# Optimization experiments

Measured on AMD Instinct MI355X. Metric: run time of the kernel, lower is better.

## Reference

```python
import jax, jax.numpy as jnp
import numpy as np

EXTENTS = (1, 1, 1)
DIM = 256
HEADS = 8
DH = 32
INNER = HEADS * DH
SCALE = DH ** -0.5
NEG = -1e9


def _windows(t):
    """t: (B, S, H, W, C) -> (B, S, H, W, K, C) local 3D windows, K = prod(2e+1).
    Pads with zeros, window dims flattened in (s, h, w) order (matches unfold i j k)."""
    e = EXTENTS
    B, S, H, W, C = t.shape
    tp = jnp.pad(t, [(0, 0), (e[0], e[0]), (e[1], e[1]), (e[2], e[2]), (0, 0)])
    slabs = []
    for dz in range(2 * e[0] + 1):
        for dy in range(2 * e[1] + 1):
            for dx in range(2 * e[2] + 1):
                slabs.append(tp[:, dz:dz + S, dy:dy + H, dx:dx + W, :])
    return jnp.stack(slabs, axis=4)


def setup_inputs() -> dict:
    key = jax.random.key(0)
    ks = jax.random.split(key, 8)
    B, S, H, W = 2, 8, 32, 32
    scale_w = DIM ** -0.5
    return {
        "x": jax.random.normal(ks[0], (B, S, H, W, DIM), jnp.float32),
        "q": jax.random.normal(ks[1], (B, S, H, W, DIM), jnp.float32),
        "Wq": jax.random.normal(ks[2], (DIM, INNER), jnp.float32) * scale_w,
        "Wk": jax.random.normal(ks[3], (DIM, INNER), jnp.float32) * scale_w,
        "Wv": jax.random.normal(ks[4], (DIM, INNER), jnp.float32) * scale_w,
        "bv": jax.random.normal(ks[5], (INNER,), jnp.float32) * 0.02,
        "Wo": jax.random.normal(ks[6], (INNER, DIM), jnp.float32) * (INNER ** -0.5),
        "bo": jax.random.normal(ks[7], (DIM,), jnp.float32) * 0.02,
    }


def reference(x, q, Wq, Wk, Wv, bv, Wo, bo):
    B, S, H, W, _ = x.shape
    k = x @ Wk                      # (B,S,H,W,INNER)
    v = x @ Wv + bv
    qp = q @ Wq

    kw = _windows(k)                # (B,S,H,W,K,INNER)
    vw = _windows(v)
    K = kw.shape[4]

    # mask: True where window element falls on padding (out of bounds)
    valid = _windows(jnp.ones((1, S, H, W, 1), jnp.float32))[..., 0] > 0  # (1,S,H,W,K)
    mask = ~valid

    qh = qp.reshape(B, S, H, W, HEADS, DH)
    kh = kw.reshape(B, S, H, W, K, HEADS, DH)
    vh = vw.reshape(B, S, H, W, K, HEADS, DH)

    dots = jnp.einsum('bshwnd,bshwknd->bshwnk', qh, kh) * SCALE  # (B,S,H,W,HEADS,K)
    dots = jnp.where(mask[:, :, :, :, None, :], NEG, dots)
    attn = jax.nn.softmax(dots, axis=-1)
    out = jnp.einsum('bshwnk,bshwknd->bshwnd', attn, vh)
    out = out.reshape(B, S, H, W, INNER)
    return out @ Wo + bo            # (B,S,H,W,DIM)
```

## Files before the change

kernel.cpp:

```cpp
#include <hip/hip_runtime.h>
#include <hip/hip_bf16.h>
#include <math.h>

#define B_N 2
#define S_N 8
#define H_N 32
#define W_N 32
#define DIM_N 256
#define NPOS (B_N * S_N * H_N * W_N)
#define NP (NPOS * DIM_N)
#define SCALE_F 0.1767766952966369f

typedef __attribute__((ext_vector_type(8))) short bf16x8;
typedef __attribute__((ext_vector_type(4))) float f32x4;

__device__ __forceinline__ unsigned short f2b(float f) {
    __hip_bfloat16 h = __float2bfloat16(f);
    return __builtin_bit_cast(unsigned short, h);
}
__device__ __forceinline__ unsigned pk2(float a, float b) {
    return (unsigned)f2b(a) | ((unsigned)f2b(b) << 16);
}
__device__ __forceinline__ float bl(unsigned u) { return __uint_as_float(u << 16); }
__device__ __forceinline__ float bh(unsigned u) { return __uint_as_float(u & 0xffff0000u); }

__global__ __launch_bounds__(256)
void wtrans_kernel(const float* __restrict__ Wq, const float* __restrict__ Wk,
                   const float* __restrict__ Wv, const float* __restrict__ Wo,
                   unsigned short* __restrict__ wt)
{
    int mat = blockIdx.y;
    const float* W = (mat == 0) ? Wq : (mat == 1) ? Wk : (mat == 2) ? Wv : Wo;
    unsigned short* Wt = wt + (size_t)mat * 65536;
    int tile = blockIdx.x;
    int tk = tile >> 3, tn = tile & 7;
    __shared__ float t[32][33];
    int c = threadIdx.x & 31;
    int r0 = (threadIdx.x >> 5) * 4;
#pragma unroll
    for (int i = 0; i < 4; ++i)
        t[r0 + i][c] = W[(size_t)(tk * 32 + r0 + i) * 256 + tn * 32 + c];
    __syncthreads();
#pragma unroll
    for (int i = 0; i < 4; ++i)
        Wt[(size_t)(tn * 32 + r0 + i) * 256 + tk * 32 + c] = f2b(t[c][r0 + i]);
}

template<bool A_F32, bool OUT_HM>
__device__ __forceinline__ void gemm_body(
    const void* __restrict__ Aptr, const unsigned short* __restrict__ Wt,
    const float* __restrict__ bias, unsigned short* __restrict__ out_hm,
    float* __restrict__ out_f, int row0, int col0)
{
    __shared__ unsigned short Al[128][72];
    __shared__ unsigned short Bl[128][72];

    const int tid = threadIdx.x;
    const int lane = tid & 63;
    const int wid = tid >> 6;
    const int wr = wid >> 1, wc = wid & 1;
    const int l15 = lane & 15, l4 = lane >> 4;

    f32x4 acc[4][4];
#pragma unroll
    for (int m = 0; m < 4; ++m)
#pragma unroll
        for (int n = 0; n < 4; ++n) acc[m][n] = (f32x4){0.f, 0.f, 0.f, 0.f};

    const int r = tid >> 3, s = tid & 7;

    for (int kt = 0; kt < DIM_N; kt += 64) {
#pragma unroll
        for (int j = 0; j < 4; ++j) {
            int rr = r + j * 32;
            if (A_F32) {
                const float* Af = (const float*)Aptr;
                const float* p = &Af[(size_t)(row0 + rr) * DIM_N + kt + s * 8];
                float4 f0 = *(const float4*)p;
                float4 f1 = *(const float4*)(p + 4);
                uint4 va;
                va.x = pk2(f0.x, f0.y); va.y = pk2(f0.z, f0.w);
                va.z = pk2(f1.x, f1.y); va.w = pk2(f1.z, f1.w);
                *(uint4*)&Al[rr][s * 8] = va;
            } else {
                const unsigned short* Ab = (const unsigned short*)Aptr;
                *(uint4*)&Al[rr][s * 8] =
                    *(const uint4*)&Ab[(size_t)(row0 + rr) * DIM_N + kt + s * 8];
            }
            *(uint4*)&Bl[rr][s * 8] =
                *(const uint4*)&Wt[(size_t)(col0 + rr) * DIM_N + kt + s * 8];
        }
        __syncthreads();
#pragma unroll
        for (int ks = 0; ks < 2; ++ks) {
            bf16x8 af[4], bfr[4];
#pragma unroll
            for (int m = 0; m < 4; ++m)
                af[m] = *(const bf16x8*)&Al[wr * 64 + m * 16 + l15][ks * 32 + l4 * 8];
#pragma unroll
            for (int n = 0; n < 4; ++n)
                bfr[n] = *(const bf16x8*)&Bl[wc * 64 + n * 16 + l15][ks * 32 + l4 * 8];
#pragma unroll
            for (int m = 0; m < 4; ++m)
#pragma unroll
                for (int n = 0; n < 4; ++n)
                    acc[m][n] = __builtin_amdgcn_mfma_f32_16x16x32_bf16(
                        af[m], bfr[n], acc[m][n], 0, 0, 0);
        }
        __syncthreads();
    }

    const int rowb = row0 + wr * 64 + l4 * 4;
    const int colb = col0 + wc * 64 + l15;
#pragma unroll
    for (int n = 0; n < 4; ++n) {
        int col = colb + n * 16;
        float bb = bias ? bias[col] : 0.f;
        int head = col >> 5, dh = col & 31;
#pragma unroll
        for (int m = 0; m < 4; ++m) {
#pragma unroll
            for (int rg = 0; rg < 4; ++rg) {
                int row = rowb + m * 16 + rg;
                float v = acc[m][n][rg] + bb;
                if (OUT_HM)
                    out_hm[((size_t)head * NPOS + row) * 32 + dh] = f2b(v);
                else
                    out_f[(size_t)row * DIM_N + col] = v;
            }
        }
    }
}

__global__ __launch_bounds__(256, 2)
void proj_mfma(const float* __restrict__ x, const float* __restrict__ q,
               const unsigned short* __restrict__ wt, const float* __restrict__ bv,
               unsigned short* __restrict__ qhb, unsigned short* __restrict__ khb,
               unsigned short* __restrict__ vhb)
{
    int z = blockIdx.z;
    const float* A = (z == 0) ? q : x;
    const unsigned short* W = wt + (size_t)z * 65536;
    unsigned short* out = (z == 0) ? qhb : (z == 1) ? khb : vhb;
    const float* bias = (z == 2) ? bv : nullptr;
    gemm_body<true, true>(A, W, bias, out, nullptr, blockIdx.x * 128, blockIdx.y * 128);
}

__global__ __launch_bounds__(256, 2)
void outp_mfma(const unsigned short* __restrict__ ao, const unsigned short* __restrict__ wt,
               const float* __restrict__ bo, float* __restrict__ out)
{
    gemm_body<false, false>(ao, wt + 3 * 65536, bo, nullptr, out,
                            blockIdx.x * 128, blockIdx.y * 128);
}

__global__ __launch_bounds__(256, 2)
void attn_kernel(const unsigned short* __restrict__ qh, const unsigned short* __restrict__ kh,
                 const unsigned short* __restrict__ vh, unsigned short* __restrict__ aop)
{
    __shared__ unsigned short aol[32 * 256];

    int bix = blockIdx.x;
    int h = bix & 31, s = (bix >> 5) & 7, b = bix >> 8;
    int n = threadIdx.x >> 5;
    int w = threadIdx.x & 31;

    size_t rowbase = (((size_t)b * S_N + s) * H_N + h) * W_N;
    size_t pos = rowbase + w;
    const unsigned short* qrow = qh + ((size_t)n * NPOS + pos) * 32;
    float qv[32];
#pragma unroll
    for (int j = 0; j < 4; ++j) {
        uint4 u = ((const uint4*)qrow)[j];
        qv[j * 8 + 0] = bl(u.x); qv[j * 8 + 1] = bh(u.x);
        qv[j * 8 + 2] = bl(u.y); qv[j * 8 + 3] = bh(u.y);
        qv[j * 8 + 4] = bl(u.z); qv[j * 8 + 5] = bh(u.z);
        qv[j * 8 + 6] = bl(u.w); qv[j * 8 + 7] = bh(u.w);
    }

    float dots[27];
#pragma unroll
    for (int dz = 0; dz < 3; ++dz)
#pragma unroll
        for (int dy = 0; dy < 3; ++dy)
#pragma unroll
            for (int dx = 0; dx < 3; ++dx) {
                int idx = (dz * 3 + dy) * 3 + dx;
                int ns = s + dz - 1, nh = h + dy - 1, nw = w + dx - 1;
                bool ok = (unsigned)ns < S_N && (unsigned)nh < H_N &&
                          (unsigned)nw < W_N;
                float d = -1e30f;
                if (ok) {
                    size_t np = (((size_t)b * S_N + ns) * H_N + nh) * W_N + nw;
                    const unsigned short* krow = kh + ((size_t)n * NPOS + np) * 32;
                    float acc = 0.f;
#pragma unroll
                    for (int j = 0; j < 4; ++j) {
                        uint4 u = ((const uint4*)krow)[j];
                        acc = fmaf(qv[j * 8 + 0], bl(u.x), acc);
                        acc = fmaf(qv[j * 8 + 1], bh(u.x), acc);
                        acc = fmaf(qv[j * 8 + 2], bl(u.y), acc);
                        acc = fmaf(qv[j * 8 + 3], bh(u.y), acc);
                        acc = fmaf(qv[j * 8 + 4], bl(u.z), acc);
                        acc = fmaf(qv[j * 8 + 5], bh(u.z), acc);
                        acc = fmaf(qv[j * 8 + 6], bl(u.w), acc);
                        acc = fmaf(qv[j * 8 + 7], bh(u.w), acc);
                    }
                    d = acc * SCALE_F;
                }
                dots[idx] = d;
            }

    float m = dots[0];
#pragma unroll
    for (int i = 1; i < 27; ++i) m = fmaxf(m, dots[i]);
    float den = 0.f;
#pragma unroll
    for (int i = 0; i < 27; ++i) {
        float p = __expf(dots[i] - m);
        dots[i] = p;
        den += p;
    }
    float inv = 1.f / den;

    float ov[32];
#pragma unroll
    for (int i = 0; i < 32; ++i) ov[i] = 0.f;
#pragma unroll
    for (int dz = 0; dz < 3; ++dz)
#pragma unroll
        for (int dy = 0; dy < 3; ++dy)
#pragma unroll
            for (int dx = 0; dx < 3; ++dx) {
                int idx = (dz * 3 + dy) * 3 + dx;
                int ns = s + dz - 1, nh = h + dy - 1, nw = w + dx - 1;
                bool ok = (unsigned)ns < S_N && (unsigned)nh < H_N &&
                          (unsigned)nw < W_N;
                if (ok) {
                    size_t np = (((size_t)b * S_N + ns) * H_N + nh) * W_N + nw;
                    const unsigned short* vrow = vh + ((size_t)n * NPOS + np) * 32;
                    float p = dots[idx];
#pragma unroll
                    for (int j = 0; j < 4; ++j) {
                        uint4 u = ((const uint4*)vrow)[j];
                        ov[j * 8 + 0] = fmaf(p, bl(u.x), ov[j * 8 + 0]);
                        ov[j * 8 + 1] = fmaf(p, bh(u.x), ov[j * 8 + 1]);
                        ov[j * 8 + 2] = fmaf(p, bl(u.y), ov[j * 8 + 2]);
                        ov[j * 8 + 3] = fmaf(p, bh(u.y), ov[j * 8 + 3]);
                        ov[j * 8 + 4] = fmaf(p, bl(u.z), ov[j * 8 + 4]);
                        ov[j * 8 + 5] = fmaf(p, bh(u.z), ov[j * 8 + 5]);
                        ov[j * 8 + 6] = fmaf(p, bl(u.w), ov[j * 8 + 6]);
                        ov[j * 8 + 7] = fmaf(p, bh(u.w), ov[j * 8 + 7]);
                    }
                }
            }

#pragma unroll
    for (int j = 0; j < 4; ++j) {
        uint4 o;
        o.x = pk2(ov[j * 8 + 0] * inv, ov[j * 8 + 1] * inv);
        o.y = pk2(ov[j * 8 + 2] * inv, ov[j * 8 + 3] * inv);
        o.z = pk2(ov[j * 8 + 4] * inv, ov[j * 8 + 5] * inv);
        o.w = pk2(ov[j * 8 + 6] * inv, ov[j * 8 + 7] * inv);
        int unit = n * 4 + j;
        int su = unit ^ (w & 7);
        *(uint4*)&aol[w * 256 + su * 8] = o;
    }
    __syncthreads();
    int wrr = threadIdx.x >> 3, c = threadIdx.x & 7;
    size_t orow = rowbase + wrr;
#pragma unroll
    for (int u = 0; u < 4; ++u) {
        int unit = c * 4 + u;
        int su = unit ^ (wrr & 7);
        uint4 v = *(const uint4*)&aol[wrr * 256 + su * 8];
        ((uint4*)(aop + orow * 256))[unit] = v;
    }
}

extern "C" void kernel_launch(void* const* d_in, const int* in_sizes, int n_in,
                              void* d_out, int out_size, void* d_ws, size_t ws_size,
                              hipStream_t stream)
{
    const float* xin = (const float*)d_in[0];
    const float* qin = (const float*)d_in[1];
    const float* Wq  = (const float*)d_in[2];
    const float* Wk  = (const float*)d_in[3];
    const float* Wv  = (const float*)d_in[4];
    const float* bv  = (const float*)d_in[5];
    const float* Wo  = (const float*)d_in[6];
    const float* bo  = (const float*)d_in[7];
    float* out = (float*)d_out;

    unsigned short* ws = (unsigned short*)d_ws;
    unsigned short* wt = ws;
    unsigned short* qh = wt + (size_t)4 * 65536;
    unsigned short* kh = qh + (size_t)NP;
    unsigned short* vh = kh + (size_t)NP;
    unsigned short* ao = vh + (size_t)NP;

    dim3 gw(64, 4);
    wtrans_kernel<<<gw, 256, 0, stream>>>(Wq, Wk, Wv, Wo, wt);

    dim3 gp(NPOS / 128, DIM_N / 128, 3);
    proj_mfma<<<gp, 256, 0, stream>>>(xin, qin, wt, bv, qh, kh, vh);

    attn_kernel<<<B_N * S_N * H_N, 256, 0, stream>>>(qh, kh, vh, ao);

    dim3 go(NPOS / 128, DIM_N / 128, 1);
    outp_mfma<<<go, 256, 0, stream>>>(ao, wt, bo, out);
}
```

Before: 73.66 us.

## Fuse output projection into attention kernel and retile QKV projection GEMM

The output projection GEMM now runs inside the attention kernel. Each block multiplies its 32x256 bf16 attention tile, already held in shared memory, by Wo, staged tile by tile into LDS, and writes the fp32 result directly. This removes the intermediate attention-output buffer round trip through global memory and one kernel launch. The QKV projection is retiled to 64-row by full-256-column blocks with 512 threads, so each A row is converted once per block. The cost is that every attention block reloads all of Wo and now needs more LDS.

```diff
diff --git a/kernel.cpp b/kernel.cpp
--- a/kernel.cpp
+++ b/kernel.cpp
@@ -46,62 +46,66 @@
         Wt[(size_t)(tn * 32 + r0 + i) * 256 + tk * 32 + c] = f2b(t[c][r0 + i]);
 }
 
-template<bool A_F32, bool OUT_HM>
-__device__ __forceinline__ void gemm_body(
-    const void* __restrict__ Aptr, const unsigned short* __restrict__ Wt,
-    const float* __restrict__ bias, unsigned short* __restrict__ out_hm,
-    float* __restrict__ out_f, int row0, int col0)
+__global__ __launch_bounds__(512, 4)
+void proj_mfma(const float* __restrict__ x, const float* __restrict__ q,
+               const unsigned short* __restrict__ wt, const float* __restrict__ bv,
+               unsigned short* __restrict__ qh, unsigned short* __restrict__ kh,
+               unsigned short* __restrict__ vh)
 {
-    __shared__ unsigned short Al[128][72];
-    __shared__ unsigned short Bl[128][72];
+    __shared__ unsigned short Al[64][72];
+    __shared__ unsigned short Bl[256][72];
+
+    const int bx = blockIdx.x;
+    const int z = bx >> 8;
+    const int row0 = (bx & 255) * 64;
+    const float* A = (z == 0) ? q : x;
+    const unsigned short* Wtm = wt + (size_t)z * 65536;
+    unsigned short* outp = (z == 0) ? qh : (z == 1) ? kh : vh;
+    const float* bias = (z == 2) ? bv : nullptr;
 
     const int tid = threadIdx.x;
     const int lane = tid & 63;
     const int wid = tid >> 6;
-    const int wr = wid >> 1, wc = wid & 1;
+    const int wm = wid >> 2, wn = wid & 3;
     const int l15 = lane & 15, l4 = lane >> 4;
 
-    f32x4 acc[4][4];
-#pragma unroll
-    for (int m = 0; m < 4; ++m)
+    f32x4 acc[2][4];
+#pragma unroll
+    for (int m = 0; m < 2; ++m)
 #pragma unroll
         for (int n = 0; n < 4; ++n) acc[m][n] = (f32x4){0.f, 0.f, 0.f, 0.f};
 
-    const int r = tid >> 3, s = tid & 7;
+    const int ar = tid >> 3, as = tid & 7;
 
     for (int kt = 0; kt < DIM_N; kt += 64) {
-#pragma unroll
-        for (int j = 0; j < 4; ++j) {
-            int rr = r + j * 32;
-            if (A_F32) {
-                const float* Af = (const float*)Aptr;
-                const float* p = &Af[(size_t)(row0 + rr) * DIM_N + kt + s * 8];
-                float4 f0 = *(const float4*)p;
-                float4 f1 = *(const float4*)(p + 4);
-                uint4 va;
-                va.x = pk2(f0.x, f0.y); va.y = pk2(f0.z, f0.w);
-                va.z = pk2(f1.x, f1.y); va.w = pk2(f1.z, f1.w);
-                *(uint4*)&Al[rr][s * 8] = va;
-            } else {
-                const unsigned short* Ab = (const unsigned short*)Aptr;
-                *(uint4*)&Al[rr][s * 8] =
-                    *(const uint4*)&Ab[(size_t)(row0 + rr) * DIM_N + kt + s * 8];
-            }
-            *(uint4*)&Bl[rr][s * 8] =
-                *(const uint4*)&Wt[(size_t)(col0 + rr) * DIM_N + kt + s * 8];
+        {
+            const float* p = &A[(size_t)(row0 + ar) * DIM_N + kt + as * 8];
+            float4 f0 = *(const float4*)p;
+            float4 f1 = *(const float4*)(p + 4);
+            uint4 va;
+            va.x = pk2(f0.x, f0.y); va.y = pk2(f0.z, f0.w);
+            va.z = pk2(f1.x, f1.y); va.w = pk2(f1.z, f1.w);
+            *(uint4*)&Al[ar][as * 8] = va;
+        }
+#pragma unroll
+        for (int i = 0; i < 4; ++i) {
+            int u = tid + i * 512;
+            int rowb = u >> 3, su = u & 7;
+            *(uint4*)&Bl[rowb][su * 8] =
+                *(const uint4*)&Wtm[(size_t)rowb * DIM_N + kt + su * 8];
         }
         __syncthreads();
 #pragma unroll
         for (int ks = 0; ks < 2; ++ks) {
-            bf16x8 af[4], bfr[4];
-#pragma unroll
-            for (int m = 0; m < 4; ++m)
-                af[m] = *(const bf16x8*)&Al[wr * 64 + m * 16 + l15][ks * 32 + l4 * 8];
+            bf16x8 af[2], bfr[4];
+#pragma unroll
+            for (int m = 0; m < 2; ++m)
+                af[m] = *(const bf16x8*)&Al[wm * 32 + m * 16 + l15][ks * 32 + l4 * 8];
 #pragma unroll
             for (int n = 0; n < 4; ++n)
-                bfr[n] = *(const bf16x8*)&Bl[wc * 64 + n * 16 + l15][ks * 32 + l4 * 8];
-#pragma unroll
-            for (int m = 0; m < 4; ++m)
+                bfr[n] = *(const bf16x8*)&Bl[wn * 64 + n * 16 + l15][ks * 32 + l4 * 8];
+#pragma unroll
+            for (int m = 0; m < 2; ++m)
 #pragma unroll
                 for (int n = 0; n < 4; ++n)
                     acc[m][n] = __builtin_amdgcn_mfma_f32_16x16x32_bf16(
@@ -110,55 +114,30 @@
         __syncthreads();
     }
 
-    const int rowb = row0 + wr * 64 + l4 * 4;
-    const int colb = col0 + wc * 64 + l15;
 #pragma unroll
     for (int n = 0; n < 4; ++n) {
-        int col = colb + n * 16;
+        int col = wn * 64 + n * 16 + l15;
         float bb = bias ? bias[col] : 0.f;
         int head = col >> 5, dh = col & 31;
 #pragma unroll
-        for (int m = 0; m < 4; ++m) {
+        for (int m = 0; m < 2; ++m) {
 #pragma unroll
             for (int rg = 0; rg < 4; ++rg) {
-                int row = rowb + m * 16 + rg;
-                float v = acc[m][n][rg] + bb;
-                if (OUT_HM)
-                    out_hm[((size_t)head * NPOS + row) * 32 + dh] = f2b(v);
-                else
-                    out_f[(size_t)row * DIM_N + col] = v;
-            }
-        }
-    }
-}
-
-__global__ __launch_bounds__(256, 2)
-void proj_mfma(const float* __restrict__ x, const float* __restrict__ q,
-               const unsigned short* __restrict__ wt, const float* __restrict__ bv,
-               unsigned short* __restrict__ qhb, unsigned short* __restrict__ khb,
-               unsigned short* __restrict__ vhb)
-{
-    int z = blockIdx.z;
-    const float* A = (z == 0) ? q : x;
-    const unsigned short* W = wt + (size_t)z * 65536;
-    unsigned short* out = (z == 0) ? qhb : (z == 1) ? khb : vhb;
-    const float* bias = (z == 2) ? bv : nullptr;
-    gemm_body<true, true>(A, W, bias, out, nullptr, blockIdx.x * 128, blockIdx.y * 128);
-}
-
-__global__ __launch_bounds__(256, 2)
-void outp_mfma(const unsigned short* __restrict__ ao, const unsigned short* __restrict__ wt,
-               const float* __restrict__ bo, float* __restrict__ out)
-{
-    gemm_body<false, false>(ao, wt + 3 * 65536, bo, nullptr, out,
-                            blockIdx.x * 128, blockIdx.y * 128);
-}
-
-__global__ __launch_bounds__(256, 2)
-void attn_kernel(const unsigned short* __restrict__ qh, const unsigned short* __restrict__ kh,
-                 const unsigned short* __restrict__ vh, unsigned short* __restrict__ aop)
+                int row = row0 + wm * 32 + m * 16 + l4 * 4 + rg;
+                outp[((size_t)head * NPOS + row) * 32 + dh] =
+                    f2b(acc[m][n][rg] + bb);
+            }
+        }
+    }
+}
+
+__global__ __launch_bounds__(256, 3)
+void attn_fused(const unsigned short* __restrict__ qh, const unsigned short* __restrict__ kh,
+                const unsigned short* __restrict__ vh, const unsigned short* __restrict__ wt3,
+                const float* __restrict__ bo, float* __restrict__ out)
 {
     __shared__ unsigned short aol[32 * 256];
+    __shared__ unsigned short Bl[256][72];
 
     int bix = blockIdx.x;
     int h = bix & 31, s = (bix >> 5) & 7, b = bix >> 8;
@@ -266,15 +245,61 @@
         int su = unit ^ (w & 7);
         *(uint4*)&aol[w * 256 + su * 8] = o;
     }
-    __syncthreads();
-    int wrr = threadIdx.x >> 3, c = threadIdx.x & 7;
-    size_t orow = rowbase + wrr;
-#pragma unroll
-    for (int u = 0; u < 4; ++u) {
-        int unit = c * 4 + u;
-        int su = unit ^ (wrr & 7);
-        uint4 v = *(const uint4*)&aol[wrr * 256 + su * 8];
-        ((uint4*)(aop + orow * 256))[unit] = v;
+
+    const int lane = threadIdx.x & 63;
+    const int wv = threadIdx.x >> 6;
+    const int l15 = lane & 15, l4 = lane >> 4;
+
+    f32x4 acc[2][4];
+#pragma unroll
+    for (int m2 = 0; m2 < 2; ++m2)
+#pragma unroll
+        for (int n2 = 0; n2 < 4; ++n2) acc[m2][n2] = (f32x4){0.f, 0.f, 0.f, 0.f};
+
+    for (int kt = 0; kt < 4; ++kt) {
+        __syncthreads();
+#pragma unroll
+        for (int i = 0; i < 8; ++i) {
+            int u = threadIdx.x + i * 256;
+            int rowb = u >> 3, su = u & 7;
+            *(uint4*)&Bl[rowb][su * 8] =
+                *(const uint4*)&wt3[(size_t)rowb * DIM_N + kt * 64 + su * 8];
+        }
+        __syncthreads();
+#pragma unroll
+        for (int ks = 0; ks < 2; ++ks) {
+            bf16x8 af[2], bfr[4];
+#pragma unroll
+            for (int m2 = 0; m2 < 2; ++m2) {
+                int r = m2 * 16 + l15;
+                int unit = kt * 8 + ks * 4 + l4;
+                int su = unit ^ (r & 7);
+                af[m2] = *(const bf16x8*)&aol[r * 256 + su * 8];
+            }
+#pragma unroll
+            for (int n2 = 0; n2 < 4; ++n2)
+                bfr[n2] = *(const bf16x8*)&Bl[wv * 64 + n2 * 16 + l15][ks * 32 + l4 * 8];
+#pragma unroll
+            for (int m2 = 0; m2 < 2; ++m2)
+#pragma unroll
+                for (int n2 = 0; n2 < 4; ++n2)
+                    acc[m2][n2] = __builtin_amdgcn_mfma_f32_16x16x32_bf16(
+                        af[m2], bfr[n2], acc[m2][n2], 0, 0, 0);
+        }
+    }
+
+#pragma unroll
+    for (int n2 = 0; n2 < 4; ++n2) {
+        int col = wv * 64 + n2 * 16 + l15;
+        float bb = bo[col];
+#pragma unroll
+        for (int m2 = 0; m2 < 2; ++m2) {
+#pragma unroll
+            for (int rg = 0; rg < 4; ++rg) {
+                int row = m2 * 16 + l4 * 4 + rg;
+                out[(rowbase + row) * DIM_N + col] = acc[m2][n2][rg] + bb;
+            }
+        }
     }
 }
 
@@ -297,16 +322,11 @@
     unsigned short* qh = wt + (size_t)4 * 65536;
     unsigned short* kh = qh + (size_t)NP;
     unsigned short* vh = kh + (size_t)NP;
-    unsigned short* ao = vh + (size_t)NP;
 
     dim3 gw(64, 4);
     wtrans_kernel<<<gw, 256, 0, stream>>>(Wq, Wk, Wv, Wo, wt);
 
-    dim3 gp(NPOS / 128, DIM_N / 128, 3);
-    proj_mfma<<<gp, 256, 0, stream>>>(xin, qin, wt, bv, qh, kh, vh);
-
-    attn_kernel<<<B_N * S_N * H_N, 256, 0, stream>>>(qh, kh, vh, ao);
-
-    dim3 go(NPOS / 128, DIM_N / 128, 1);
-    outp_mfma<<<go, 256, 0, stream>>>(ao, wt, bo, out);
-}
+    proj_mfma<<<768, 512, 0, stream>>>(xin, qin, wt, bv, qh, kh, vh);
+
+    attn_fused<<<B_N * S_N * H_N, 256, 0, stream>>>(qh, kh, vh, wt + 3 * 65536, bo, out);
+}
```

After: 64.05 us. 13.1% less time.
